# Kernel tuning notes

Measured on AMD Instinct MI355X. Metric: run time of the kernel, lower is better.

Reference implementation:

```python
import jax, jax.numpy as jnp
import numpy as np

D = 1024
D_PRE_HEAD = 128
H = 16
D_ROPE = D_PRE_HEAD // 2          # 64
DC_V = D_PRE_HEAD                 # 128
DC_KV = D_PRE_HEAD // 8           # 16
DC_Q = D // 4                     # 256
Q_HEAD_DIM = D_PRE_HEAD + D_ROPE  # 192
MEG_D = D_PRE_HEAD + DC_V         # 256
MAX_LEN = 8192
EPS = 1e-7


def rms_norm(x, w):
    x32 = x.astype(jnp.float32)
    var = jnp.mean(x32 * x32, axis=-1, keepdims=True)
    return w * (x32 * jax.lax.rsqrt(var + EPS)).astype(x.dtype)


def rope_cos_sin():
    inv_freq = 1.0 / (10000.0 ** (jnp.arange(0, D_ROPE, 2, dtype=jnp.float32) / D_ROPE))
    freqs = jnp.outer(jnp.arange(MAX_LEN, dtype=jnp.float32), inv_freq)
    emb = jnp.concatenate([freqs, freqs], axis=-1)  # [MAX_LEN, D_ROPE]
    return jnp.cos(emb), jnp.sin(emb)


def rope_reshape(x):
    # view(...,d//2,2).transpose(-1,-2).reshape == concat(even, odd) along last dim
    return jnp.concatenate([x[..., 0::2], x[..., 1::2]], axis=-1)


def rope_rotate(x):
    h = x.shape[-1] // 2
    return jnp.concatenate([-x[..., h:], x[..., :h]], axis=-1)


def setup_inputs() -> dict:
    key = jax.random.key(0)
    ks = jax.random.split(key, 12)
    B, SQ, SKV = 2, 2048, 2048
    s = 0.02
    return {
        "q_inputs": jax.random.normal(ks[0], (B, SQ, D), jnp.float32),
        "kv_input": jax.random.normal(ks[1], (B, SKV, D), jnp.float32),
        "q_pos_ids": jax.random.randint(ks[2], (B, SQ), 0, MAX_LEN),
        "kv_pos_ids": jax.random.randint(ks[3], (B, SKV), 0, MAX_LEN),
        # weights stored as [in, out] (torch Linear weight transposed)
        "Wq_down": jax.random.normal(ks[4], (D, DC_Q), jnp.float32) * s,
        "q_norm_w": jnp.ones((DC_Q,), jnp.float32),
        "Wq_up": jax.random.normal(ks[5], (DC_Q, H * Q_HEAD_DIM), jnp.float32) * s,
        "Wkv_down": jax.random.normal(ks[6], (D, DC_KV + D_ROPE), jnp.float32) * s,
        "kv_norm_w": jnp.ones((DC_KV,), jnp.float32),
        "Wkv_up": jax.random.normal(ks[7], (DC_KV, H * MEG_D), jnp.float32) * s,
        "Wout": jax.random.normal(ks[8], (H * DC_V, D), jnp.float32) * s,
    }


def reference(q_inputs, kv_input, q_pos_ids, kv_pos_ids,
              Wq_down, q_norm_w, Wq_up, Wkv_down, kv_norm_w, Wkv_up, Wout):
    B, SQ, _ = q_inputs.shape
    SKV = kv_input.shape[1]

    # query path: low-rank down -> RMSNorm -> up
    q = rms_norm(q_inputs @ Wq_down, q_norm_w) @ Wq_up
    q = q.reshape(B, SQ, H, Q_HEAD_DIM).transpose(0, 2, 1, 3)  # [B,H,SQ,192]
    q_nope, q_rope = q[..., :D_PRE_HEAD], q[..., D_PRE_HEAD:]

    # kv path: compressed latent + decoupled rope slice
    ckv_full = kv_input @ Wkv_down                              # [B,SKV,DC_KV+D_ROPE]
    c_kv, k_rope = ckv_full[..., :DC_KV], ckv_full[..., DC_KV:]
    c_kv = rms_norm(c_kv, kv_norm_w)
    kv = (c_kv @ Wkv_up).reshape(B, SKV, H, MEG_D).transpose(0, 2, 1, 3)
    k_nope, value = kv[..., :D_PRE_HEAD], kv[..., D_PRE_HEAD:]  # [B,H,SKV,128] each
    k_rope = k_rope[:, None, :, :]                              # [B,1,SKV,64]

    # RoPE with per-token position ids
    cos, sin = rope_cos_sin()
    q_cos, q_sin = cos[q_pos_ids][:, None], sin[q_pos_ids][:, None]   # [B,1,SQ,64]
    k_cos, k_sin = cos[kv_pos_ids][:, None], sin[kv_pos_ids][:, None]
    qr = rope_reshape(q_rope)
    kr = rope_reshape(k_rope)
    q_rope = qr * q_cos + rope_rotate(qr) * q_sin
    k_rope = kr * k_cos + rope_rotate(kr) * k_sin

    query = jnp.concatenate([q_nope, q_rope], axis=-1)                         # [B,H,SQ,192]
    key_t = jnp.concatenate([k_nope, jnp.broadcast_to(k_rope, (B, H, SKV, D_ROPE))], axis=-1)

    scale = 1.0 / jnp.sqrt(jnp.asarray(Q_HEAD_DIM, query.dtype))
    scores = jnp.einsum('bhqd,bhkd->bhqk', query, key_t) * scale
    attn = jax.nn.softmax(scores, axis=-1)
    out = jnp.einsum('bhqk,bhkd->bhqd', attn, value)                           # [B,H,SQ,128]
    out = out.transpose(0, 2, 1, 3).reshape(B, SQ, H * DC_V)
    return out @ Wout
```

## Files before the change

### kernel.cpp

```cpp
#include <hip/hip_runtime.h>

typedef unsigned short u16;
typedef unsigned int u32;
typedef u16 u16x4 __attribute__((ext_vector_type(4)));
typedef u16 u16x8 __attribute__((ext_vector_type(8)));
typedef float f32x4 __attribute__((ext_vector_type(4)));
typedef __bf16 bf16x8 __attribute__((ext_vector_type(8)));

#define DEV static __device__ __forceinline__

DEV float bf2f(u16 u) { u32 v = ((u32)u) << 16; float f; __builtin_memcpy(&f, &v, 4); return f; }
DEV u16 f2bf(float f) { u32 v; __builtin_memcpy(&v, &f, 4); v += 0x7fffu + ((v >> 16) & 1u); return (u16)(v >> 16); }
DEV bf16x8 ld_frag(const u16* p) { u16x8 v = *(const u16x8*)p; return __builtin_bit_cast(bf16x8, v); }

#define LOG10000 9.210340372f

__global__ __launch_bounds__(256) void k_cvt(const float* __restrict__ in, u16* __restrict__ out) {
  size_t i = ((size_t)blockIdx.x * 256 + threadIdx.x) * 8;
  f32x4 a = *(const f32x4*)(in + i);
  f32x4 b = *(const f32x4*)(in + i + 4);
  u16x8 o = { f2bf(a[0]), f2bf(a[1]), f2bf(a[2]), f2bf(a[3]),
              f2bf(b[0]), f2bf(b[1]), f2bf(b[2]), f2bf(b[3]) };
  *(u16x8*)(out + i) = o;
}

__global__ __launch_bounds__(256) void k_wtrans(const float* __restrict__ in, u16* __restrict__ out,
                                                int R, int C, int Rp) {
  __shared__ float tile[32][33];
  int c0 = blockIdx.x * 32, r0 = blockIdx.y * 32;
  int tx = threadIdx.x & 31, ty = threadIdx.x >> 5;
#pragma unroll
  for (int p = 0; p < 4; p++) {
    int r = r0 + ty + p * 8, c = c0 + tx;
    tile[ty + p * 8][tx] = (r < R && c < C) ? in[(size_t)r * C + c] : 0.f;
  }
  __syncthreads();
#pragma unroll
  for (int p = 0; p < 4; p++)
    out[(size_t)(c0 + ty + p * 8) * Rp + r0 + tx] = f2bf(tile[tx][ty + p * 8]);
}

template <int OUT_BF16>
__global__ __launch_bounds__(256) void k_gemm(const u16* __restrict__ A, const u16* __restrict__ Bt,
                                              void* __restrict__ Cv, int M, int N, int K) {
  constexpr int LSTR = 40;
  __shared__ u16 As[128 * LSTR], Bs[128 * LSTR];
  const int tid = threadIdx.x, l = tid & 63, w = tid >> 6;
  const int nwg = gridDim.x * gridDim.y;
  const int lin = blockIdx.y * gridDim.x + blockIdx.x;
  const int swzb = (lin & 7) * (nwg >> 3) + (lin >> 3);
  const int m0 = (swzb / gridDim.x) * 128, n0 = (swzb % gridDim.x) * 128;
  const int wr = (w >> 1) * 64, wc = (w & 1) * 64;
  const int lr = l & 15, lk = (l >> 4) * 8;
  const int sr = tid >> 2, sc = (tid & 3) * 8;
  f32x4 acc[4][4] = {};
  const u16* pa0 = A + (size_t)(m0 + sr) * K + sc;
  const u16* pa1 = A + (size_t)(m0 + 64 + sr) * K + sc;
  const u16* pb0 = Bt + (size_t)(n0 + sr) * K + sc;
  const u16* pb1 = Bt + (size_t)(n0 + 64 + sr) * K + sc;
  u16x8 va0 = *(const u16x8*)pa0, va1 = *(const u16x8*)pa1;
  u16x8 vb0 = *(const u16x8*)pb0, vb1 = *(const u16x8*)pb1;
  for (int k0 = 0; k0 < K; k0 += 32) {
    *(u16x8*)&As[sr * LSTR + sc] = va0;
    *(u16x8*)&As[(64 + sr) * LSTR + sc] = va1;
    *(u16x8*)&Bs[sr * LSTR + sc] = vb0;
    *(u16x8*)&Bs[(64 + sr) * LSTR + sc] = vb1;
    __syncthreads();
    if (k0 + 32 < K) {
      va0 = *(const u16x8*)(pa0 + k0 + 32);
      va1 = *(const u16x8*)(pa1 + k0 + 32);
      vb0 = *(const u16x8*)(pb0 + k0 + 32);
      vb1 = *(const u16x8*)(pb1 + k0 + 32);
    }
    bf16x8 af[4], bf[4];
#pragma unroll
    for (int i = 0; i < 4; i++) af[i] = ld_frag(&As[(wr + i * 16 + lr) * LSTR + lk]);
#pragma unroll
    for (int j = 0; j < 4; j++) bf[j] = ld_frag(&Bs[(wc + j * 16 + lr) * LSTR + lk]);
#pragma unroll
    for (int i = 0; i < 4; i++)
#pragma unroll
      for (int j = 0; j < 4; j++)
        acc[i][j] = __builtin_amdgcn_mfma_f32_16x16x32_bf16(af[i], bf[j], acc[i][j], 0, 0, 0);
    __syncthreads();
  }
#pragma unroll
  for (int i = 0; i < 4; i++)
#pragma unroll
    for (int j = 0; j < 4; j++) {
      int row = m0 + wr + i * 16 + (l >> 4) * 4;
      int col = n0 + wc + j * 16 + lr;
#pragma unroll
      for (int r = 0; r < 4; r++) {
        if (OUT_BF16) ((u16*)Cv)[(size_t)(row + r) * N + col] = f2bf(acc[i][j][r]);
        else          ((float*)Cv)[(size_t)(row + r) * N + col] = acc[i][j][r];
      }
    }
}

template <int OUT_BF16>
__global__ __launch_bounds__(256) void k_gemmh(const u16* __restrict__ A, const u16* __restrict__ Bt,
                                               void* __restrict__ Cv, int M, int N, int K) {
  constexpr int LSTR = 40;
  __shared__ u16 As[64 * LSTR], Bs[128 * LSTR];
  const int tid = threadIdx.x, l = tid & 63, w = tid >> 6;
  const int nwg = gridDim.x * gridDim.y;
  const int lin = blockIdx.y * gridDim.x + blockIdx.x;
  const int swzb = (lin & 7) * (nwg >> 3) + (lin >> 3);
  const int m0 = (swzb / gridDim.x) * 64, n0 = (swzb % gridDim.x) * 128;
  const int wr = (w >> 1) * 32, wc = (w & 1) * 64;
  const int lr = l & 15, lk = (l >> 4) * 8;
  const int sr = tid >> 2, sc = (tid & 3) * 8;
  f32x4 acc[2][4] = {};
  const u16* pa0 = A + (size_t)(m0 + sr) * K + sc;
  const u16* pb0 = Bt + (size_t)(n0 + sr) * K + sc;
  const u16* pb1 = Bt + (size_t)(n0 + 64 + sr) * K + sc;
  u16x8 va0 = *(const u16x8*)pa0;
  u16x8 vb0 = *(const u16x8*)pb0, vb1 = *(const u16x8*)pb1;
  for (int k0 = 0; k0 < K; k0 += 32) {
    *(u16x8*)&As[sr * LSTR + sc] = va0;
    *(u16x8*)&Bs[sr * LSTR + sc] = vb0;
    *(u16x8*)&Bs[(64 + sr) * LSTR + sc] = vb1;
    __syncthreads();
    if (k0 + 32 < K) {
      va0 = *(const u16x8*)(pa0 + k0 + 32);
      vb0 = *(const u16x8*)(pb0 + k0 + 32);
      vb1 = *(const u16x8*)(pb1 + k0 + 32);
    }
    bf16x8 af[2], bf[4];
#pragma unroll
    for (int i = 0; i < 2; i++) af[i] = ld_frag(&As[(wr + i * 16 + lr) * LSTR + lk]);
#pragma unroll
    for (int j = 0; j < 4; j++) bf[j] = ld_frag(&Bs[(wc + j * 16 + lr) * LSTR + lk]);
#pragma unroll
    for (int i = 0; i < 2; i++)
#pragma unroll
      for (int j = 0; j < 4; j++)
        acc[i][j] = __builtin_amdgcn_mfma_f32_16x16x32_bf16(af[i], bf[j], acc[i][j], 0, 0, 0);
    __syncthreads();
  }
#pragma unroll
  for (int i = 0; i < 2; i++)
#pragma unroll
    for (int j = 0; j < 4; j++) {
      int row = m0 + wr + i * 16 + (l >> 4) * 4;
      int col = n0 + wc + j * 16 + lr;
#pragma unroll
      for (int r = 0; r < 4; r++) {
        if (OUT_BF16) ((u16*)Cv)[(size_t)(row + r) * N + col] = f2bf(acc[i][j][r]);
        else          ((float*)Cv)[(size_t)(row + r) * N + col] = acc[i][j][r];
      }
    }
}

template <int OUT_BF16>
__global__ __launch_bounds__(256) void k_gemm64(const u16* __restrict__ A, const u16* __restrict__ Bt,
                                                void* __restrict__ Cv, int M, int N, int K) {
  constexpr int LSTR = 40;
  __shared__ u16 As[64 * LSTR], Bs[64 * LSTR];
  const int tid = threadIdx.x, l = tid & 63, w = tid >> 6;
  const int nwg = gridDim.x * gridDim.y;
  const int lin = blockIdx.y * gridDim.x + blockIdx.x;
  const int swzb = (lin & 7) * (nwg >> 3) + (lin >> 3);
  const int m0 = (swzb / gridDim.x) * 64, n0 = (swzb % gridDim.x) * 64;
  const int wr = (w >> 1) * 32, wc = (w & 1) * 32;
  const int lr = l & 15, lk = (l >> 4) * 8;
  const int sr = tid >> 2, sc = (tid & 3) * 8;
  f32x4 acc[2][2] = {};
  const u16* pa0 = A + (size_t)(m0 + sr) * K + sc;
  const u16* pb0 = Bt + (size_t)(n0 + sr) * K + sc;
  u16x8 va0 = *(const u16x8*)pa0;
  u16x8 vb0 = *(const u16x8*)pb0;
  for (int k0 = 0; k0 < K; k0 += 32) {
    *(u16x8*)&As[sr * LSTR + sc] = va0;
    *(u16x8*)&Bs[sr * LSTR + sc] = vb0;
    __syncthreads();
    if (k0 + 32 < K) {
      va0 = *(const u16x8*)(pa0 + k0 + 32);
      vb0 = *(const u16x8*)(pb0 + k0 + 32);
    }
    bf16x8 af[2], bf[2];
#pragma unroll
    for (int i = 0; i < 2; i++) af[i] = ld_frag(&As[(wr + i * 16 + lr) * LSTR + lk]);
#pragma unroll
    for (int j = 0; j < 2; j++) bf[j] = ld_frag(&Bs[(wc + j * 16 + lr) * LSTR + lk]);
#pragma unroll
    for (int i = 0; i < 2; i++)
#pragma unroll
      for (int j = 0; j < 2; j++)
        acc[i][j] = __builtin_amdgcn_mfma_f32_16x16x32_bf16(af[i], bf[j], acc[i][j], 0, 0, 0);
    __syncthreads();
  }
#pragma unroll
  for (int i = 0; i < 2; i++)
#pragma unroll
    for (int j = 0; j < 2; j++) {
      int row = m0 + wr + i * 16 + (l >> 4) * 4;
      int col = n0 + wc + j * 16 + lr;
#pragma unroll
      for (int r = 0; r < 4; r++) {
        if (OUT_BF16) ((u16*)Cv)[(size_t)(row + r) * N + col] = f2bf(acc[i][j][r]);
        else          ((float*)Cv)[(size_t)(row + r) * N + col] = acc[i][j][r];
      }
    }
}

__global__ __launch_bounds__(64) void k_kvnorm(const float* __restrict__ ckvf, const float* __restrict__ nw,
                                               const int* __restrict__ pos, u16* __restrict__ ckvn,
                                               u16* __restrict__ kropeb) {
  int row = blockIdx.x, l = threadIdx.x;
  const float* x = ckvf + (size_t)row * 128;
  float v = (l < 16) ? x[l] : 0.f;
  float ss = v * v;
  ss += __shfl_xor(ss, 1); ss += __shfl_xor(ss, 2); ss += __shfl_xor(ss, 4); ss += __shfl_xor(ss, 8);
  if (l < 16) ckvn[(size_t)row * 32 + l] = f2bf(v * rsqrtf(ss * (1.f / 16.f) + 1e-7f) * nw[l]);
  if (l >= 16 && l < 32) ckvn[(size_t)row * 32 + l] = 0;
  if (l < 32) {
    float invf = __expf(-(LOG10000 / 32.f) * (float)l);
    float ang = (float)pos[row] * invf;
    float c = cosf(ang), s = sinf(ang);
    float e = x[16 + 2 * l], o = x[17 + 2 * l];
    kropeb[(size_t)row * 64 + l]      = f2bf(e * c - o * s);
    kropeb[(size_t)row * 64 + l + 32] = f2bf(o * c + e * s);
  }
}

__global__ __launch_bounds__(256) void k_rms256(const float* __restrict__ in, const float* __restrict__ w,
                                                u16* __restrict__ out, float scale) {
  int row = blockIdx.x * 4 + (threadIdx.x >> 6);
  int l = threadIdx.x & 63;
  const float* x = in + (size_t)row * 256;
  f32x4 v = *(const f32x4*)(x + l * 4);
  float ss = v[0] * v[0] + v[1] * v[1] + v[2] * v[2] + v[3] * v[3];
#pragma unroll
  for (int m = 1; m < 64; m <<= 1) ss += __shfl_xor(ss, m);
  float rinv = rsqrtf(ss * (1.f / 256.f) + 1e-7f) * scale;
  const f32x4 wv = *(const f32x4*)(w + l * 4);
  u16x4 o = { f2bf(v[0] * rinv * wv[0]), f2bf(v[1] * rinv * wv[1]),
              f2bf(v[2] * rinv * wv[2]), f2bf(v[3] * rinv * wv[3]) };
  *(u16x4*)(out + (size_t)row * 256 + l * 4) = o;
}

__global__ __launch_bounds__(256) void k_qrope(u16* __restrict__ q, const int* __restrict__ pos) {
  __shared__ float cs[32], sn[32];
  int bs = blockIdx.x, tid = threadIdx.x;
  if (tid < 32) {
    float invf = __expf(-(LOG10000 / 32.f) * (float)tid);
    float ang = (float)pos[bs] * invf;
    cs[tid] = cosf(ang); sn[tid] = sinf(ang);
  }
  __syncthreads();
  u16* base = q + (size_t)bs * 3072;
  int h0 = tid >> 5, p0 = tid & 31;
  int h1 = h0 + 8, p1 = p0;
  u16* r0p = base + h0 * 192 + 128;
  u16* r1p = base + h1 * 192 + 128;
  float e0 = bf2f(r0p[2 * p0]), o0 = bf2f(r0p[2 * p0 + 1]);
  float e1 = bf2f(r1p[2 * p1]), o1 = bf2f(r1p[2 * p1 + 1]);
  __syncthreads();
  r0p[p0]      = f2bf(e0 * cs[p0] - o0 * sn[p0]);
  r0p[p0 + 32] = f2bf(o0 * cs[p0] + e0 * sn[p0]);
  r1p[p1]      = f2bf(e1 * cs[p1] - o1 * sn[p1]);
  r1p[p1 + 32] = f2bf(o1 * cs[p1] + e1 * sn[p1]);
}

__global__ void k_vt(const u16* __restrict__ Ckv, u16* __restrict__ VT) {
  __shared__ u16 tile[32][40];
  int bh = blockIdx.z, b = bh >> 4, h = bh & 15;
  int d0 = blockIdx.x * 32, s0 = blockIdx.y * 32;
  int tx = threadIdx.x, ty = threadIdx.y;
  const u16* src = Ckv + ((size_t)(b * 2048 + s0)) * 4096 + h * 256 + 128 + d0;
#pragma unroll
  for (int p = 0; p < 4; p++) tile[ty + p * 8][tx] = src[(size_t)(ty + p * 8) * 4096 + tx];
  __syncthreads();
  u16* dst = VT + ((size_t)bh * 128 + d0) * 2048 + s0;
#pragma unroll
  for (int p = 0; p < 4; p++) dst[(size_t)(ty + p * 8) * 2048 + tx] = tile[tx][ty + p * 8];
}

__global__ __launch_bounds__(512, 2) void k_attn(const u16* __restrict__ Qp, const u16* __restrict__ Ckv,
                                                 const u16* __restrict__ kropeb, const u16* __restrict__ VT,
                                                 u16* __restrict__ AO) {
  __shared__ u16 Ks[64 * 192];
  __shared__ u16 Vs[128 * 64];
  __shared__ u16 Ps[128 * 64];
  const int tid = threadIdx.x, l = tid & 63, w = tid >> 6;
  const int lr = l & 15, h4 = l >> 4, lk = h4 * 8;
  const int bid = blockIdx.x, bh = bid & 31, qt = bid >> 5;
  const int b = bh >> 4, hh = bh & 15;
  const int m0 = qt * 128;
  const u32 swz = (u32)(lr & 7) << 3;

  bf16x8 qa[6];
  {
    const u16* qrow = Qp + (size_t)(b * 2048 + m0 + w * 16 + lr) * 3072 + hh * 192;
#pragma unroll
    for (int kk = 0; kk < 6; kk++) qa[kk] = ld_frag(qrow + kk * 32 + lk);
  }

  const u16* kptr[3]; int kstep[3]; u32 klds[3];
#pragma unroll
  for (int p = 0; p < 3; p++) {
    int c2 = tid + p * 512;
    int r = c2 / 24, cc = c2 - r * 24;
    klds[p] = (u32)(r * 192 + cc * 8) ^ ((u32)(r & 7) << 3);
    if (cc < 16) { kptr[p] = Ckv + ((size_t)(b * 2048 + r)) * 4096 + hh * 256 + cc * 8; kstep[p] = 64 * 4096; }
    else         { kptr[p] = kropeb + ((size_t)(b * 2048 + r)) * 64 + (cc - 16) * 8;    kstep[p] = 64 * 64; }
  }
  const u16* vptr[2]; u32 vlds[2];
#pragma unroll
  for (int p = 0; p < 2; p++) {
    int c2 = tid + p * 512;
    int d = c2 >> 3, cc = c2 & 7;
    vlds[p] = (u32)(d * 64 + cc * 8) ^ ((u32)(d & 7) << 3);
    vptr[p] = VT + ((size_t)bh * 128 + d) * 2048 + cc * 8;
  }
  u16x8 kreg[3], vreg[2];
#pragma unroll
  for (int p = 0; p < 3; p++) { kreg[p] = *(const u16x8*)kptr[p]; kptr[p] += kstep[p]; }
#pragma unroll
  for (int p = 0; p < 2; p++) { vreg[p] = *(const u16x8*)vptr[p]; vptr[p] += 64; }

  f32x4 oacc[8] = {};
  float lsum[4] = {};
  const int odd = l & 1;

  for (int t = 0; t < 32; t++) {
#pragma unroll
    for (int p = 0; p < 3; p++) *(u16x8*)&Ks[klds[p]] = kreg[p];
#pragma unroll
    for (int p = 0; p < 2; p++) *(u16x8*)&Vs[vlds[p]] = vreg[p];
    __syncthreads();
    if (t + 1 < 32) {
#pragma unroll
      for (int p = 0; p < 3; p++) { kreg[p] = *(const u16x8*)kptr[p]; kptr[p] += kstep[p]; }
#pragma unroll
      for (int p = 0; p < 2; p++) { vreg[p] = *(const u16x8*)vptr[p]; vptr[p] += 64; }
    }
    f32x4 sacc[4] = {};
    __builtin_amdgcn_s_setprio(1);
#pragma unroll
    for (int n = 0; n < 4; n++)
#pragma unroll
      for (int kk = 0; kk < 6; kk++)
        sacc[n] = __builtin_amdgcn_mfma_f32_16x16x32_bf16(
            qa[kk], ld_frag(&Ks[(u32)((n * 16 + lr) * 192 + kk * 32 + lk) ^ swz]), sacc[n], 0, 0, 0);
    __builtin_amdgcn_s_setprio(0);
    const int prow = w * 16 + 4 * h4;
#pragma unroll
    for (int n = 0; n < 4; n++) {
      float o0 = __expf(sacc[n][0]), o1 = __expf(sacc[n][1]),
            o2 = __expf(sacc[n][2]), o3 = __expf(sacc[n][3]);
      lsum[0] += o0; lsum[1] += o1; lsum[2] += o2; lsum[3] += o3;
      float p0 = __shfl_xor(o0, 1), p1 = __shfl_xor(o1, 1),
            p2 = __shfl_xor(o2, 1), p3 = __shfl_xor(o3, 1);
      float lo0 = odd ? p2 : o0, hi0 = odd ? o2 : p0;
      float lo1 = odd ? p3 : o1, hi1 = odd ? o3 : p1;
      int r0 = odd ? 2 : 0;
      u32 w0 = (u32)f2bf(lo0) | ((u32)f2bf(hi0) << 16);
      u32 w1 = (u32)f2bf(lo1) | ((u32)f2bf(hi1) << 16);
      int col = n * 16 + (lr & ~1);
      int row0 = prow + r0, row1 = prow + r0 + 1;
      *(u32*)&Ps[(u32)(row0 * 64 + col) ^ ((u32)(row0 & 7) << 3)] = w0;
      *(u32*)&Ps[(u32)(row1 * 64 + col) ^ ((u32)(row1 & 7) << 3)] = w1;
    }
    __builtin_amdgcn_s_setprio(1);
#pragma unroll
    for (int kk = 0; kk < 2; kk++) {
      bf16x8 pa = ld_frag(&Ps[(u32)((w * 16 + lr) * 64 + kk * 32 + lk) ^ swz]);
#pragma unroll
      for (int n2 = 0; n2 < 8; n2++)
        oacc[n2] = __builtin_amdgcn_mfma_f32_16x16x32_bf16(
            pa, ld_frag(&Vs[(u32)((n2 * 16 + lr) * 64 + kk * 32 + lk) ^ swz]), oacc[n2], 0, 0, 0);
    }
    __builtin_amdgcn_s_setprio(0);
    __syncthreads();
  }
  float rl[4];
#pragma unroll
  for (int r = 0; r < 4; r++) {
    float s = lsum[r];
    s += __shfl_xor(s, 1); s += __shfl_xor(s, 2); s += __shfl_xor(s, 4); s += __shfl_xor(s, 8);
    rl[r] = 1.f / s;
  }
#pragma unroll
  for (int n2 = 0; n2 < 8; n2++)
#pragma unroll
    for (int r = 0; r < 4; r++) {
      int row = m0 + w * 16 + h4 * 4 + r;
      AO[((size_t)(b * 2048 + row) * 16 + hh) * 128 + n2 * 16 + lr] = f2bf(oacc[n2][r] * rl[r]);
    }
}

extern "C" void kernel_launch(void* const* d_in, const int* in_sizes, int n_in,
                              void* d_out, int out_size, void* d_ws, size_t ws_size,
                              hipStream_t stream) {
  const float* q_in  = (const float*)d_in[0];
  const float* kv_in = (const float*)d_in[1];
  const int*   qpos  = (const int*)d_in[2];
  const int*   kpos  = (const int*)d_in[3];
  const float* Wqd   = (const float*)d_in[4];
  const float* qnw   = (const float*)d_in[5];
  const float* Wqu   = (const float*)d_in[6];
  const float* Wkvd  = (const float*)d_in[7];
  const float* kvnw  = (const float*)d_in[8];
  const float* Wkvu  = (const float*)d_in[9];
  const float* Wo    = (const float*)d_in[10];
  float* out = (float*)d_out;
  char* ws = (char*)d_ws;
  size_t off = 0;
  auto alloc = [&](size_t bytes) -> void* {
    void* p = ws + off; off += (bytes + 255) & ~(size_t)255; return p;
  };
  u16*   Aq     = (u16*)alloc(4096ull * 1024 * 2);
  u16*   Akv    = (u16*)alloc(4096ull * 1024 * 2);
  u16*   WqdT   = (u16*)alloc(256ull * 1024 * 2);
  u16*   WquT   = (u16*)alloc(3072ull * 256 * 2);
  u16*   WkvdT  = (u16*)alloc(128ull * 1024 * 2);
  u16*   WkvuT  = (u16*)alloc(4096ull * 32 * 2);
  u16*   WoT    = (u16*)alloc(1024ull * 2048 * 2);
  float* ckvf   = (float*)alloc(4096ull * 128 * 4);
  u16*   ckvn   = (u16*)alloc(4096ull * 32 * 2);
  u16*   kropeb = (u16*)alloc(4096ull * 64 * 2);
  u16*   Ckv    = (u16*)alloc(4096ull * 4096 * 2);
  u16*   VTb    = (u16*)alloc(32ull * 128 * 2048 * 2);
  float* cq     = (float*)alloc(4096ull * 256 * 4);
  u16*   cqn    = (u16*)alloc(4096ull * 256 * 2);
  u16*   qproj  = (u16*)alloc(4096ull * 3072 * 2);
  u16*   AOb    = (u16*)alloc(4096ull * 2048 * 2);
  (void)in_sizes; (void)n_in; (void)out_size; (void)ws_size;

  k_cvt<<<2048, 256, 0, stream>>>(q_in, Aq);
  k_cvt<<<2048, 256, 0, stream>>>(kv_in, Akv);
  k_wtrans<<<dim3(8, 32), 256, 0, stream>>>(Wqd, WqdT, 1024, 256, 1024);
  k_wtrans<<<dim3(96, 8), 256, 0, stream>>>(Wqu, WquT, 256, 3072, 256);
  k_wtrans<<<dim3(4, 32), 256, 0, stream>>>(Wkvd, WkvdT, 1024, 80, 1024);
  k_wtrans<<<dim3(128, 1), 256, 0, stream>>>(Wkvu, WkvuT, 16, 4096, 32);
  k_wtrans<<<dim3(32, 64), 256, 0, stream>>>(Wo, WoT, 2048, 1024, 2048);
  k_gemm64<0><<<dim3(2, 64), 256, 0, stream>>>(Akv, WkvdT, ckvf, 4096, 128, 1024);
  k_kvnorm<<<4096, 64, 0, stream>>>(ckvf, kvnw, kpos, ckvn, kropeb);
  k_gemm<1><<<dim3(32, 32), 256, 0, stream>>>(ckvn, WkvuT, Ckv, 4096, 4096, 32);
  k_vt<<<dim3(4, 64, 32), dim3(32, 8), 0, stream>>>(Ckv, VTb);
  k_gemm64<0><<<dim3(4, 64), 256, 0, stream>>>(Aq, WqdT, cq, 4096, 256, 1024);
  k_rms256<<<1024, 256, 0, stream>>>(cq, qnw, cqn, 0.07216878364870322f);
  k_gemm<1><<<dim3(24, 32), 256, 0, stream>>>(cqn, WquT, qproj, 4096, 3072, 256);
  k_qrope<<<4096, 256, 0, stream>>>(qproj, qpos);
  k_attn<<<512, 512, 0, stream>>>(qproj, Ckv, kropeb, VTb, AOb);
  k_gemmh<0><<<dim3(8, 64), 256, 0, stream>>>(AOb, WoT, out, 4096, 1024, 2048);
}
```

Before: 259.5 us.

## Fuse fp32-to-bf16 conversion into down-proj GEMMs, vectorize V transpose, keep P in registers

Removes the two standalone input conversion kernels by loading fp32 activations directly in the down-projection GEMM and converting to bf16 while staging into LDS. The V transpose kernel switches to 64x64 tiles with 16-byte vector loads and stores. In attention, the QK MFMA operands are swapped so each lane holds a column of scores. The probabilities are then rearranged into PV A-fragments with cross-lane shuffles instead of a round trip through shared memory, which also simplifies the row-sum reduction. The cost is more shuffle instructions and more fp32 global traffic inside the GEMM.

Measured after the change: 259.3 us. No clear change (-0.1%).

```diff
diff --git a/kernel.cpp b/kernel.cpp
--- a/kernel.cpp
+++ b/kernel.cpp
@@ -4,6 +4,7 @@
 typedef unsigned int u32;
 typedef u16 u16x4 __attribute__((ext_vector_type(4)));
 typedef u16 u16x8 __attribute__((ext_vector_type(8)));
+typedef u32 u32x4 __attribute__((ext_vector_type(4)));
 typedef float f32x4 __attribute__((ext_vector_type(4)));
 typedef __bf16 bf16x8 __attribute__((ext_vector_type(8)));
 
@@ -14,15 +15,6 @@
 DEV bf16x8 ld_frag(const u16* p) { u16x8 v = *(const u16x8*)p; return __builtin_bit_cast(bf16x8, v); }
 
 #define LOG10000 9.210340372f
-
-__global__ __launch_bounds__(256) void k_cvt(const float* __restrict__ in, u16* __restrict__ out) {
-  size_t i = ((size_t)blockIdx.x * 256 + threadIdx.x) * 8;
-  f32x4 a = *(const f32x4*)(in + i);
-  f32x4 b = *(const f32x4*)(in + i + 4);
-  u16x8 o = { f2bf(a[0]), f2bf(a[1]), f2bf(a[2]), f2bf(a[3]),
-              f2bf(b[0]), f2bf(b[1]), f2bf(b[2]), f2bf(b[3]) };
-  *(u16x8*)(out + i) = o;
-}
 
 __global__ __launch_bounds__(256) void k_wtrans(const float* __restrict__ in, u16* __restrict__ out,
                                                 int R, int C, int Rp) {
@@ -154,8 +146,8 @@
 }
 
 template <int OUT_BF16>
-__global__ __launch_bounds__(256) void k_gemm64(const u16* __restrict__ A, const u16* __restrict__ Bt,
-                                                void* __restrict__ Cv, int M, int N, int K) {
+__global__ __launch_bounds__(256) void k_gemm64f(const float* __restrict__ A, const u16* __restrict__ Bt,
+                                                 void* __restrict__ Cv, int M, int N, int K) {
   constexpr int LSTR = 40;
   __shared__ u16 As[64 * LSTR], Bs[64 * LSTR];
   const int tid = threadIdx.x, l = tid & 63, w = tid >> 6;
@@ -167,16 +159,19 @@
   const int lr = l & 15, lk = (l >> 4) * 8;
   const int sr = tid >> 2, sc = (tid & 3) * 8;
   f32x4 acc[2][2] = {};
-  const u16* pa0 = A + (size_t)(m0 + sr) * K + sc;
+  const float* pa0 = A + (size_t)(m0 + sr) * K + sc;
   const u16* pb0 = Bt + (size_t)(n0 + sr) * K + sc;
-  u16x8 va0 = *(const u16x8*)pa0;
+  f32x4 vaa = *(const f32x4*)pa0, vab = *(const f32x4*)(pa0 + 4);
   u16x8 vb0 = *(const u16x8*)pb0;
   for (int k0 = 0; k0 < K; k0 += 32) {
+    u16x8 va0 = { f2bf(vaa[0]), f2bf(vaa[1]), f2bf(vaa[2]), f2bf(vaa[3]),
+                  f2bf(vab[0]), f2bf(vab[1]), f2bf(vab[2]), f2bf(vab[3]) };
     *(u16x8*)&As[sr * LSTR + sc] = va0;
     *(u16x8*)&Bs[sr * LSTR + sc] = vb0;
     __syncthreads();
     if (k0 + 32 < K) {
-      va0 = *(const u16x8*)(pa0 + k0 + 32);
+      vaa = *(const f32x4*)(pa0 + k0 + 32);
+      vab = *(const f32x4*)(pa0 + k0 + 36);
       vb0 = *(const u16x8*)(pb0 + k0 + 32);
     }
     bf16x8 af[2], bf[2];
@@ -264,18 +259,27 @@
   r1p[p1 + 32] = f2bf(o1 * cs[p1] + e1 * sn[p1]);
 }
 
-__global__ void k_vt(const u16* __restrict__ Ckv, u16* __restrict__ VT) {
-  __shared__ u16 tile[32][40];
+__global__ __launch_bounds__(256) void k_vt(const u16* __restrict__ Ckv, u16* __restrict__ VT) {
+  __shared__ u16 tile[64][72];
   int bh = blockIdx.z, b = bh >> 4, h = bh & 15;
-  int d0 = blockIdx.x * 32, s0 = blockIdx.y * 32;
-  int tx = threadIdx.x, ty = threadIdx.y;
-  const u16* src = Ckv + ((size_t)(b * 2048 + s0)) * 4096 + h * 256 + 128 + d0;
-#pragma unroll
-  for (int p = 0; p < 4; p++) tile[ty + p * 8][tx] = src[(size_t)(ty + p * 8) * 4096 + tx];
+  int d0 = blockIdx.x * 64, s0 = blockIdx.y * 64;
+  int tid = threadIdx.x;
+#pragma unroll
+  for (int p = 0; p < 2; p++) {
+    int c = tid + p * 256;
+    int r = c >> 3, cc = (c & 7) * 8;
+    *(u16x8*)&tile[r][cc] =
+        *(const u16x8*)&Ckv[((size_t)(b * 2048 + s0 + r)) * 4096 + h * 256 + 128 + d0 + cc];
+  }
   __syncthreads();
-  u16* dst = VT + ((size_t)bh * 128 + d0) * 2048 + s0;
-#pragma unroll
-  for (int p = 0; p < 4; p++) dst[(size_t)(ty + p * 8) * 2048 + tx] = tile[tx][ty + p * 8];
+#pragma unroll
+  for (int p = 0; p < 2; p++) {
+    int c = tid + p * 256;
+    int d = c >> 3, ss = (c & 7) * 8;
+    u16x8 v = { tile[ss][d],     tile[ss + 1][d], tile[ss + 2][d], tile[ss + 3][d],
+                tile[ss + 4][d], tile[ss + 5][d], tile[ss + 6][d], tile[ss + 7][d] };
+    *(u16x8*)&VT[((size_t)bh * 128 + d0 + d) * 2048 + s0 + ss] = v;
+  }
 }
 
 __global__ __launch_bounds__(512, 2) void k_attn(const u16* __restrict__ Qp, const u16* __restrict__ Ckv,
@@ -283,9 +287,8 @@
                                                  u16* __restrict__ AO) {
   __shared__ u16 Ks[64 * 192];
   __shared__ u16 Vs[128 * 64];
-  __shared__ u16 Ps[128 * 64];
   const int tid = threadIdx.x, l = tid & 63, w = tid >> 6;
-  const int lr = l & 15, h4 = l >> 4, lk = h4 * 8;
+  const int lr = l & 15, g = l >> 4, lk = g * 8;
   const int bid = blockIdx.x, bh = bid & 31, qt = bid >> 5;
   const int b = bh >> 4, hh = bh & 15;
   const int m0 = qt * 128;
@@ -322,8 +325,10 @@
   for (int p = 0; p < 2; p++) { vreg[p] = *(const u16x8*)vptr[p]; vptr[p] += 64; }
 
   f32x4 oacc[8] = {};
-  float lsum[4] = {};
-  const int odd = l & 1;
+  float lsum = 0.f;
+  const int srcA = lr + ((l & 16) << 1);
+  const int srcB = srcA + 16;
+  const bool hi = (l & 32) != 0;
 
   for (int t = 0; t < 32; t++) {
 #pragma unroll
@@ -344,51 +349,55 @@
 #pragma unroll
       for (int kk = 0; kk < 6; kk++)
         sacc[n] = __builtin_amdgcn_mfma_f32_16x16x32_bf16(
-            qa[kk], ld_frag(&Ks[(u32)((n * 16 + lr) * 192 + kk * 32 + lk) ^ swz]), sacc[n], 0, 0, 0);
+            ld_frag(&Ks[(u32)((n * 16 + lr) * 192 + kk * 32 + lk) ^ swz]), qa[kk], sacc[n], 0, 0, 0);
     __builtin_amdgcn_s_setprio(0);
-    const int prow = w * 16 + 4 * h4;
+    u32 pw[4][2];
 #pragma unroll
     for (int n = 0; n < 4; n++) {
-      float o0 = __expf(sacc[n][0]), o1 = __expf(sacc[n][1]),
-            o2 = __expf(sacc[n][2]), o3 = __expf(sacc[n][3]);
-      lsum[0] += o0; lsum[1] += o1; lsum[2] += o2; lsum[3] += o3;
-      float p0 = __shfl_xor(o0, 1), p1 = __shfl_xor(o1, 1),
-            p2 = __shfl_xor(o2, 1), p3 = __shfl_xor(o3, 1);
-      float lo0 = odd ? p2 : o0, hi0 = odd ? o2 : p0;
-      float lo1 = odd ? p3 : o1, hi1 = odd ? o3 : p1;
-      int r0 = odd ? 2 : 0;
-      u32 w0 = (u32)f2bf(lo0) | ((u32)f2bf(hi0) << 16);
-      u32 w1 = (u32)f2bf(lo1) | ((u32)f2bf(hi1) << 16);
-      int col = n * 16 + (lr & ~1);
-      int row0 = prow + r0, row1 = prow + r0 + 1;
-      *(u32*)&Ps[(u32)(row0 * 64 + col) ^ ((u32)(row0 & 7) << 3)] = w0;
-      *(u32*)&Ps[(u32)(row1 * 64 + col) ^ ((u32)(row1 & 7) << 3)] = w1;
+      float p0 = __expf(sacc[n][0]), p1 = __expf(sacc[n][1]),
+            p2 = __expf(sacc[n][2]), p3 = __expf(sacc[n][3]);
+      lsum += (p0 + p1) + (p2 + p3);
+      pw[n][0] = (u32)f2bf(p0) | ((u32)f2bf(p1) << 16);
+      pw[n][1] = (u32)f2bf(p2) | ((u32)f2bf(p3) << 16);
+    }
+    u32 pa32[2][4];
+#pragma unroll
+    for (int kk2 = 0; kk2 < 2; kk2++) {
+      u32 t0a = __shfl(pw[2 * kk2][0], srcA), t1a = __shfl(pw[2 * kk2 + 1][0], srcA);
+      u32 t0b = __shfl(pw[2 * kk2][1], srcA), t1b = __shfl(pw[2 * kk2 + 1][1], srcA);
+      u32 t0c = __shfl(pw[2 * kk2][0], srcB), t1c = __shfl(pw[2 * kk2 + 1][0], srcB);
+      u32 t0d = __shfl(pw[2 * kk2][1], srcB), t1d = __shfl(pw[2 * kk2 + 1][1], srcB);
+      pa32[kk2][0] = hi ? t1a : t0a;
+      pa32[kk2][1] = hi ? t1b : t0b;
+      pa32[kk2][2] = hi ? t1c : t0c;
+      pa32[kk2][3] = hi ? t1d : t0d;
     }
     __builtin_amdgcn_s_setprio(1);
 #pragma unroll
-    for (int kk = 0; kk < 2; kk++) {
-      bf16x8 pa = ld_frag(&Ps[(u32)((w * 16 + lr) * 64 + kk * 32 + lk) ^ swz]);
+    for (int kk2 = 0; kk2 < 2; kk2++) {
+      u32x4 pv = { pa32[kk2][0], pa32[kk2][1], pa32[kk2][2], pa32[kk2][3] };
+      bf16x8 paf = __builtin_bit_cast(bf16x8, pv);
 #pragma unroll
       for (int n2 = 0; n2 < 8; n2++)
         oacc[n2] = __builtin_amdgcn_mfma_f32_16x16x32_bf16(
-            pa, ld_frag(&Vs[(u32)((n2 * 16 + lr) * 64 + kk * 32 + lk) ^ swz]), oacc[n2], 0, 0, 0);
+            paf, ld_frag(&Vs[(u32)((n2 * 16 + lr) * 64 + kk2 * 32 + lk) ^ swz]), oacc[n2], 0, 0, 0);
     }
     __builtin_amdgcn_s_setprio(0);
     __syncthreads();
   }
-  float rl[4];
-#pragma unroll
-  for (int r = 0; r < 4; r++) {
-    float s = lsum[r];
-    s += __shfl_xor(s, 1); s += __shfl_xor(s, 2); s += __shfl_xor(s, 4); s += __shfl_xor(s, 8);
-    rl[r] = 1.f / s;
-  }
+  float s = lsum;
+  s += __shfl_xor(s, 16);
+  s += __shfl_xor(s, 32);
+  float rl = 1.f / s;
+  float rlv[4];
+#pragma unroll
+  for (int r = 0; r < 4; r++) rlv[r] = __shfl(rl, g * 4 + r);
 #pragma unroll
   for (int n2 = 0; n2 < 8; n2++)
 #pragma unroll
     for (int r = 0; r < 4; r++) {
-      int row = m0 + w * 16 + h4 * 4 + r;
-      AO[((size_t)(b * 2048 + row) * 16 + hh) * 128 + n2 * 16 + lr] = f2bf(oacc[n2][r] * rl[r]);
+      int row = m0 + w * 16 + g * 4 + r;
+      AO[((size_t)(b * 2048 + row) * 16 + hh) * 128 + n2 * 16 + lr] = f2bf(oacc[n2][r] * rlv[r]);
     }
 }
 
@@ -412,8 +421,6 @@
   auto alloc = [&](size_t bytes) -> void* {
     void* p = ws + off; off += (bytes + 255) & ~(size_t)255; return p;
   };
-  u16*   Aq     = (u16*)alloc(4096ull * 1024 * 2);
-  u16*   Akv    = (u16*)alloc(4096ull * 1024 * 2);
   u16*   WqdT   = (u16*)alloc(256ull * 1024 * 2);
   u16*   WquT   = (u16*)alloc(3072ull * 256 * 2);
   u16*   WkvdT  = (u16*)alloc(128ull * 1024 * 2);
@@ -430,18 +437,16 @@
   u16*   AOb    = (u16*)alloc(4096ull * 2048 * 2);
   (void)in_sizes; (void)n_in; (void)out_size; (void)ws_size;
 
-  k_cvt<<<2048, 256, 0, stream>>>(q_in, Aq);
-  k_cvt<<<2048, 256, 0, stream>>>(kv_in, Akv);
   k_wtrans<<<dim3(8, 32), 256, 0, stream>>>(Wqd, WqdT, 1024, 256, 1024);
   k_wtrans<<<dim3(96, 8), 256, 0, stream>>>(Wqu, WquT, 256, 3072, 256);
   k_wtrans<<<dim3(4, 32), 256, 0, stream>>>(Wkvd, WkvdT, 1024, 80, 1024);
   k_wtrans<<<dim3(128, 1), 256, 0, stream>>>(Wkvu, WkvuT, 16, 4096, 32);
   k_wtrans<<<dim3(32, 64), 256, 0, stream>>>(Wo, WoT, 2048, 1024, 2048);
-  k_gemm64<0><<<dim3(2, 64), 256, 0, stream>>>(Akv, WkvdT, ckvf, 4096, 128, 1024);
+  k_gemm64f<0><<<dim3(2, 64), 256, 0, stream>>>(kv_in, WkvdT, ckvf, 4096, 128, 1024);
   k_kvnorm<<<4096, 64, 0, stream>>>(ckvf, kvnw, kpos, ckvn, kropeb);
   k_gemm<1><<<dim3(32, 32), 256, 0, stream>>>(ckvn, WkvuT, Ckv, 4096, 4096, 32);
-  k_vt<<<dim3(4, 64, 32), dim3(32, 8), 0, stream>>>(Ckv, VTb);
-  k_gemm64<0><<<dim3(4, 64), 256, 0, stream>>>(Aq, WqdT, cq, 4096, 256, 1024);
+  k_vt<<<dim3(2, 32, 32), 256, 0, stream>>>(Ckv, VTb);
+  k_gemm64f<0><<<dim3(4, 64), 256, 0, stream>>>(q_in, WqdT, cq, 4096, 256, 1024);
   k_rms256<<<1024, 256, 0, stream>>>(cq, qnw, cqn, 0.07216878364870322f);
   k_gemm<1><<<dim3(24, 32), 256, 0, stream>>>(cqn, WquT, qproj, 4096, 3072, 256);
   k_qrope<<<4096, 256, 0, stream>>>(qproj, qpos);
```
